# Optimization experiments

Measured on AMD Instinct MI355X. Metric: run time of the kernel, lower is better.

The kernel has to match this reference:

```python
import jax, jax.numpy as jnp
import numpy as np

B, N, H, NH = 1024, 101, 128, 8
HD = H // NH
EPS = 1e-5  # torch LayerNorm default


def _xavier(k, shape):
    fan_in, fan_out = shape
    lim = float(np.sqrt(6.0 / (fan_in + fan_out)))
    return jax.random.uniform(k, shape, jnp.float32, -lim, lim)


def setup_inputs() -> dict:
    key = jax.random.key(0)
    ks = jax.random.split(key, 12)
    return {
        "encoder_inputs": jax.random.normal(ks[0], (B, N, H), jnp.float32),
        "pool": jax.random.normal(ks[1], (B, H), jnp.float32),
        "capacity": jnp.ones((B, 1), jnp.float32),
        "demand": jax.random.uniform(ks[2], (B, N), jnp.float32),
        "fc_w": _xavier(ks[3], (H + 1, H)),      # nn.Linear(hidden+1, hidden, bias=False), stored [in,out]
        "fc1_w": _xavier(ks[4], (H, H)),
        "dec_ln_g": jnp.ones((H,), jnp.float32),
        "dec_ln_b": jnp.zeros((H,), jnp.float32),
        "wq": _xavier(ks[5], (H, H)),             # TransformerAttention q/k/v/out projections
        "wk": _xavier(ks[6], (H, H)),
        "wv": _xavier(ks[7], (H, H)),
        "wo": _xavier(ks[8], (H, H)),
        "kp_w": _xavier(ks[9], (H, H)),           # pointer self.k
        "ptr_ln_g": jnp.ones((H,), jnp.float32),
        "ptr_ln_b": jnp.zeros((H,), jnp.float32),
        "n_steps": 120,
        "T": 1,
        "greedy": 1,
    }


def _ln(x, g, b):
    mu = x.mean(-1, keepdims=True)
    v = ((x - mu) ** 2).mean(-1, keepdims=True)
    return (x - mu) * jax.lax.rsqrt(v + EPS) * g + b


def _forward(encoder_inputs, pool, capacity, demand, fc_w, fc1_w, dec_ln_g, dec_ln_b,
             wq, wk, wv, wo, kp_w, ptr_ln_g, ptr_ln_b, n_steps, T):
    b, n, h = encoder_inputs.shape
    # context projections are loop-invariant -> hoist out of the decode loop
    Kh = (encoder_inputs @ wk).reshape(b, n, NH, HD)
    Vh = (encoder_inputs @ wv).reshape(b, n, NH, HD)
    Kp = encoder_inputs @ kp_w            # [B,N,H] pointer keys
    pool_proc = pool @ fc1_w              # [B,H]
    ar = jnp.arange(n)
    arB = jnp.arange(b)
    inv_sqrt_hd = 1.0 / jnp.sqrt(jnp.float32(HD))
    inv_sqrt_h = 1.0 / jnp.sqrt(jnp.float32(h))

    def step(carry, i):
        mask1, cap, idx, inp = carry
        # decoder input: fc([emb, remaining_cap]) + fc1(pool), LayerNorm
        d = jnp.concatenate([inp, cap], -1) @ fc_w + pool_proc
        d = _ln(d, dec_ln_g, dec_ln_b)
        # ---- update_mask ----
        hit = (ar[None, :] == idx[:, None]) & (idx[:, None] != 0)
        mask1 = jnp.where((i > 0) & hit, 1.0, mask1)
        infeas = (mask1[:, 1:] > 0) | (demand[:, 1:] > cap)      # customers
        any_feas = jnp.any(~infeas, axis=-1)
        depot_m = jnp.where(i == 0, True, (idx == 0) & any_feas)  # mask depot if at depot & feasible cust exists
        all_cust = jnp.all(infeas, axis=-1)
        depot_m = jnp.where(all_cust, False, depot_m)             # only depot allowed if no feasible customer
        mb = jnp.concatenate([depot_m[:, None], infeas], axis=1)  # [B,N] bool, True = masked
        # ---- TransformerAttention (mhalayer) ----
        Qh = (d @ wq).reshape(b, NH, HD)
        logit = jnp.einsum('bhd,bnhd->bhn', Qh, Kh) * inv_sqrt_hd
        logit = jnp.where(mb[:, None, :], -jnp.inf, logit)
        attn = jax.nn.softmax(logit, axis=-1)
        x = jnp.einsum('bhn,bnhd->bhd', attn, Vh).reshape(b, h) @ wo
        # ---- pointer compatibility ----
        xn = _ln(x, ptr_ln_g, ptr_ln_b)
        comp = jnp.einsum('bh,bnh->bn', xn, Kp) * inv_sqrt_h
        comp = jnp.where(mb, -jnp.inf, comp)
        comp = jnp.where(jnp.all(mb, axis=-1, keepdims=True), 0.0, comp)
        p = jax.nn.softmax(comp / T, axis=-1) + 1e-10
        p = p / p.sum(axis=-1, keepdims=True)
        idx = jnp.argmax(p, axis=-1)                              # greedy selection
        lp = jnp.log(jnp.take_along_axis(p, idx[:, None], 1)[:, 0])
        done = mask1[:, 1:].sum(-1) >= (n - 1)
        lp = jnp.where(done, 0.0, lp)
        # ---- update_state (demand lookups via .item() in torch -> stop_gradient) ----
        sel = jax.lax.stop_gradient(jnp.take_along_axis(demand, idx[:, None], 1))
        cap = jnp.where(idx[:, None] == 0, jax.lax.stop_gradient(capacity), cap - sel)
        inp = encoder_inputs[arB, idx]
        return (mask1, cap, idx, inp), (idx, lp)

    init = (jnp.zeros((b, n), jnp.float32), capacity,
            jnp.zeros((b,), jnp.int32), encoder_inputs[:, 0])
    _, (idxs, lps) = jax.lax.scan(step, init, jnp.arange(n_steps))
    last = idxs[-1]
    final = jnp.where(last == 0, -1, 0).astype(jnp.int32)
    actions = jnp.concatenate(
        [jnp.zeros((b, 1), jnp.int32), idxs.T.astype(jnp.int32), final[:, None]], axis=1)
    log_p = lps.sum(0)
    return actions, log_p


def reference(encoder_inputs, pool, capacity, demand, fc_w, fc1_w, dec_ln_g, dec_ln_b,
              wq, wk, wv, wo, kp_w, ptr_ln_g, ptr_ln_b, n_steps, T, greedy):
    # greedy flag: this reference implements the greedy=True path (deterministic argmax).
    return _forward(encoder_inputs, pool, capacity, demand, fc_w, fc1_w, dec_ln_g,
                    dec_ln_b, wq, wk, wv, wo, kp_w, ptr_ln_g, ptr_ln_b,
                    int(n_steps), float(T))
```

## Files before the change

kernel.cpp:

```cpp
#include <hip/hip_runtime.h>
#include <math.h>

constexpr int N_ = 101, H_ = 128;
constexpr int SKE = 132;
constexpr float EPS_ = 1e-5f;

constexpr int OFF_TAB = 0;
constexpr int OFF_AT  = N_ * SKE;
constexpr int OFF_FC  = OFF_AT + 816;
constexpr int OFF_XV  = OFF_FC + 128;
constexpr int OFF_YR  = OFF_XV + 128;
constexpr int OFF_CP  = OFF_YR + 128;
constexpr int LDS_WORDS = OFF_CP + 128;

__device__ __forceinline__ float rdlane(float v, int l) {
  return __int_as_float(__builtin_amdgcn_readlane(__float_as_int(v), l));
}

template<int CTRL, int RM>
__device__ __forceinline__ float dppadd(float x) {
  int v = __builtin_amdgcn_update_dpp(0, __float_as_int(x), CTRL, RM, 0xf, true);
  return x + __int_as_float(v);
}
template<int CTRL, int RM>
__device__ __forceinline__ float dppmax(float x) {
  int v = __builtin_amdgcn_update_dpp(__float_as_int(x), __float_as_int(x), CTRL, RM, 0xf, false);
  return fmaxf(x, __int_as_float(v));
}
__device__ __forceinline__ float wave_sum(float x) {
  x = dppadd<0x111,0xf>(x);
  x = dppadd<0x112,0xf>(x);
  x = dppadd<0x114,0xf>(x);
  x = dppadd<0x118,0xf>(x);
  x = dppadd<0x142,0xa>(x);
  x = dppadd<0x143,0xc>(x);
  return rdlane(x, 63);
}
__device__ __forceinline__ float wave_max(float x) {
  x = dppmax<0x111,0xf>(x); x = dppmax<0x112,0xf>(x);
  x = dppmax<0x114,0xf>(x); x = dppmax<0x118,0xf>(x);
  x = dppmax<0x142,0xa>(x); x = dppmax<0x143,0xc>(x);
  return rdlane(x, 63);
}
__device__ __forceinline__ float grp4_sum(float x) {
  x = dppadd<0x111,0xf>(x);
  x = dppadd<0x112,0xf>(x);
  return x;
}

__global__ __launch_bounds__(512, 2) void gat_decoder(
    const float* __restrict__ enc, const float* __restrict__ pool,
    const float* __restrict__ capac, const float* __restrict__ dem,
    const float* __restrict__ fcw, const float* __restrict__ fc1w,
    const float* __restrict__ lng, const float* __restrict__ lnb,
    const float* __restrict__ wq, const float* __restrict__ wk,
    const float* __restrict__ wvm, const float* __restrict__ wo,
    const float* __restrict__ kpw, const float* __restrict__ plg,
    const float* __restrict__ plb, const int* __restrict__ tp,
    float* __restrict__ out, int Bv, int ns)
{
  __shared__ float sm[LDS_WORDS];
  const int tid  = threadIdx.x;
  const int b    = blockIdx.x;
  const int lane = tid & 63;
  const int wvid = tid >> 6;
  const int sl   = lane & 3;
  const int lc   = lane >> 2;
  const int col  = wvid * 16 + lc;
  const int n1 = lane, n2 = lane + 64;

  const float NEG_INF = -__builtin_inff();
  int ti = tp[0];
  float Tf = (ti > 1000000 || ti < -1000000) ? __int_as_float((int)ti) : (float)ti;
  const float inv_sqrt_h = 1.0f / sqrtf(128.0f);
  const float PSUM_CONST = 1.0f + (float)N_ * 1e-10f;

  const float* encb = enc + (size_t)b * (N_ * H_);

  float* TAB = sm + OFF_TAB;  float* AT = sm + OFF_AT;
  float* FC  = sm + OFF_FC;   float* XV = sm + OFF_XV;
  float* YR  = sm + OFF_YR;   float* CP = sm + OFF_CP;

  const int j3 = tid & 127;
  const int g3 = __builtin_amdgcn_readfirstlane(tid >> 7);
  const int r03 = g3 * 26, nr3 = (g3 == 3) ? 23 : 26;

  {
    const float* pb = pool + (size_t)b * H_;
    float p = 0.f;
    #pragma unroll
    for (int r = 0; r < 32; ++r) p = fmaf(pb[g3 * 32 + r], fc1w[(g3 * 32 + r) * H_ + j3], p);
    AT[g3 * 128 + j3] = p;
    if (tid < 128) FC[tid] = fcw[128 * H_ + tid];
  }
  __syncthreads();
  if (tid < 128) CP[tid] = AT[tid] + AT[128 + tid] + AT[256 + tid] + AT[384 + tid];

  {
    float acc[26];
    #pragma unroll
    for (int t = 0; t < 26; ++t) acc[t] = 0.f;
    for (int k0 = 0; k0 < H_; k0 += 8) {
      float w8[8];
      #pragma unroll
      for (int kk = 0; kk < 8; ++kk) w8[kk] = kpw[(k0 + kk) * H_ + j3];
      #pragma unroll
      for (int t = 0; t < 26; ++t) if (t < nr3) {
        const float* ep = encb + (r03 + t) * H_ + k0;
        #pragma unroll
        for (int kk = 0; kk < 8; ++kk) acc[t] = fmaf(ep[kk], w8[kk], acc[t]);
      }
    }
    #pragma unroll
    for (int t = 0; t < 26; ++t) if (t < nr3) TAB[(r03 + t) * SKE + j3] = acc[t];
  }
  __syncthreads();

  float kpT[32], kps, cpb;
  {
    const int neff = (col < N_) ? col : (N_ - 1);
    const float* src = TAB + neff * SKE + sl * 32;
    float ks = 0.f, cb = 0.f;
    #pragma unroll
    for (int r = 0; r < 32; ++r) {
      const float kv = src[r];
      const float pg = plg[sl * 32 + r];
      const float pb2 = plb[sl * 32 + r];
      ks = fmaf(kv, pg, ks);
      cb = fmaf(kv, pb2, cb);
      kpT[r] = kv * pg;
    }
    kps = grp4_sum(ks); cpb = grp4_sum(cb);
  }
  __syncthreads();

  {
    float acc[26];
    #pragma unroll
    for (int t = 0; t < 26; ++t) acc[t] = 0.f;
    for (int k0 = 0; k0 < H_; k0 += 8) {
      float w8[8];
      #pragma unroll
      for (int kk = 0; kk < 8; ++kk) w8[kk] = wk[(k0 + kk) * H_ + j3];
      #pragma unroll
      for (int t = 0; t < 26; ++t) if (t < nr3) {
        const float* ep = encb + (r03 + t) * H_ + k0;
        #pragma unroll
        for (int kk = 0; kk < 8; ++kk) acc[t] = fmaf(ep[kk], w8[kk], acc[t]);
      }
    }
    #pragma unroll
    for (int t = 0; t < 26; ++t) if (t < nr3) TAB[(r03 + t) * SKE + j3] = acc[t];
  }
  __syncthreads();

  float khA[16], khB[16];
  {
    const int row2 = (n2 < N_) ? n2 : n1;
    const float* s1 = TAB + n1 * SKE + wvid * 16;
    const float* s2 = TAB + row2 * SKE + wvid * 16;
    #pragma unroll
    for (int d = 0; d < 16; ++d) { khA[d] = s1[d]; khB[d] = s2[d]; }
  }
  __syncthreads();

  {
    const float pcj = CP[j3];
    float acc[26];
    #pragma unroll
    for (int t = 0; t < 26; ++t) acc[t] = pcj;
    for (int k0 = 0; k0 < H_; k0 += 8) {
      float w8[8];
      #pragma unroll
      for (int kk = 0; kk < 8; ++kk) w8[kk] = fcw[(k0 + kk) * H_ + j3];
      #pragma unroll
      for (int t = 0; t < 26; ++t) if (t < nr3) {
        const float* ep = encb + (r03 + t) * H_ + k0;
        #pragma unroll
        for (int kk = 0; kk < 8; ++kk) acc[t] = fmaf(ep[kk], w8[kk], acc[t]);
      }
    }
    #pragma unroll
    for (int t = 0; t < 26; ++t) if (t < nr3) TAB[(r03 + t) * SKE + j3] = acc[t];
  }

  float vh[26];
  {
    const int r0v = sl * 26, nrv = (sl == 3) ? 23 : 26;
    #pragma unroll
    for (int t = 0; t < 26; ++t) vh[t] = 0.f;
    for (int k0 = 0; k0 < H_; k0 += 8) {
      float w8[8];
      #pragma unroll
      for (int kk = 0; kk < 8; ++kk) w8[kk] = wvm[(k0 + kk) * H_ + col];
      #pragma unroll
      for (int t = 0; t < 26; ++t) if (t < nrv) {
        const float* ep = encb + (r0v + t) * H_ + k0;
        #pragma unroll
        for (int kk = 0; kk < 8; ++kk) vh[t] = fmaf(ep[kk], w8[kk], vh[t]);
      }
    }
  }
  float wq_r[32], wo_r[32], wqs, qb, wfc;
  {
    float ws = 0.f, bsum = 0.f, wf = 0.f;
    #pragma unroll
    for (int r = 0; r < 32; ++r) {
      wo_r[r] = wo[(sl * 32 + r) * H_ + col];
      const float w = wq[(sl * 32 + r) * H_ + col];
      const float lg = lng[sl * 32 + r];
      const float lb = lnb[sl * 32 + r];
      const float wp = w * lg;
      wq_r[r] = wp;
      ws += wp;
      bsum = fmaf(w, lb, bsum);
      wf = fmaf(wp, fcw[128 * H_ + sl * 32 + r], wf);
    }
    wqs = grp4_sum(ws); qb = grp4_sum(bsum); wfc = grp4_sum(wf);
  }
  const float capv = capac[b];
  float cap = capv, lpsum = 0.f;
  float demA = dem[(size_t)b * N_ + n1];
  float demC = (n2 < N_) ? dem[(size_t)b * N_ + n2] : 0.f;
  int vis = 0, pidx = 0;
  bool m1a = false, m1c = false, mbA, mbB;
  {
    bool infA = (n1 >= 1) && (demA > cap);
    bool infB = (n2 >= N_) || (demC > cap);
    bool feasA = (n1 >= 1) && !infA;
    bool feasB = (n2 < N_) && !infB;
    const bool anyf = __any(feasA || feasB);
    mbA = (n1 == 0) ? anyf : infA;
    mbB = infB;
  }
  __syncthreads();

  for (int i = 0; i < ns; ++i) {
    const int pu = __builtin_amdgcn_readfirstlane(pidx);
    const float* EROW = TAB + pu * SKE;

    {
      const float DA = EROW[n1] + cap * FC[n1];
      const float DC = EROW[n2 & 127] + cap * FC[n2 & 127];
      const float mu = wave_sum(DA + DC) * (1.f / 128.f);
      const float da = DA - mu, dc = DC - mu;
      const float inv = 1.0f / sqrtf(wave_sum(da * da + dc * dc) * (1.f / 128.f) + EPS_);
      const float4* e4 = (const float4*)(EROW + sl * 32);
      float p = 0.f;
      #pragma unroll
      for (int r4 = 0; r4 < 8; ++r4) {
        const float4 u = e4[r4];
        p = fmaf(wq_r[r4 * 4 + 0], u.x, p);
        p = fmaf(wq_r[r4 * 4 + 1], u.y, p);
        p = fmaf(wq_r[r4 * 4 + 2], u.z, p);
        p = fmaf(wq_r[r4 * 4 + 3], u.w, p);
      }
      p = grp4_sum(p);
      const float q = inv * ((p + cap * wfc) - mu * wqs) + qb;
      float a1 = 0.f, a2r = 0.f;
      #pragma unroll
      for (int d = 0; d < 16; ++d) {
        const float qdv = rdlane(q, 4 * d + 3);
        a1  = fmaf(qdv, khA[d], a1);
        a2r = fmaf(qdv, khB[d], a2r);
      }
      a1 = mbA ? NEG_INF : a1 * 0.25f;
      float a2 = (n2 < N_ && !mbB) ? a2r * 0.25f : NEG_INF;
      const float mx = wave_max(fmaxf(a1, a2));
      float e1 = expf(a1 - mx);
      float e2 = (n2 < N_) ? expf(a2 - mx) : 0.f;
      const float ss = wave_sum(e1 + e2);
      AT[wvid * N_ + n1] = e1 / ss;
      if (n2 < N_) AT[wvid * N_ + n2] = e2 / ss;
      const float* aw = AT + wvid * N_ + sl * 26;
      const int nrv = (sl == 3) ? 23 : 26;
      float x = 0.f;
      #pragma unroll
      for (int t = 0; t < 26; ++t) if (t < nrv) x = fmaf(aw[t], vh[t], x);
      x = grp4_sum(x);
      if (sl == 3) XV[col] = x;
    }
    __syncthreads();

    {
      const float4* xp4 = (const float4*)(XV + sl * 32);
      float y = 0.f;
      #pragma unroll
      for (int r4 = 0; r4 < 8; ++r4) {
        const float4 u = xp4[r4];
        y = fmaf(wo_r[r4 * 4 + 0], u.x, y);
        y = fmaf(wo_r[r4 * 4 + 1], u.y, y);
        y = fmaf(wo_r[r4 * 4 + 2], u.z, y);
        y = fmaf(wo_r[r4 * 4 + 3], u.w, y);
      }
      y = grp4_sum(y);
      if (sl == 3) YR[col] = y;
    }
    __syncthreads();

    {
      const float YA = YR[n1], YC = YR[n2 & 127];
      const float mu = wave_sum(YA + YC) * (1.f / 128.f);
      const float da = YA - mu, dc = YC - mu;
      const float inv = 1.0f / sqrtf(wave_sum(da * da + dc * dc) * (1.f / 128.f) + EPS_);
      const float4* yp4 = (const float4*)(YR + sl * 32);
      float c = 0.f;
      #pragma unroll
      for (int r4 = 0; r4 < 8; ++r4) {
        const float4 u = yp4[r4];
        c = fmaf(kpT[r4 * 4 + 0], u.x, c);
        c = fmaf(kpT[r4 * 4 + 1], u.y, c);
        c = fmaf(kpT[r4 * 4 + 2], u.z, c);
        c = fmaf(kpT[r4 * 4 + 3], u.w, c);
      }
      c = grp4_sum(c);
      const float comp = inv * (c - mu * kps) + cpb;
      if (sl == 3 && col < N_) CP[col] = comp;
    }
    __syncthreads();

    {
      const bool allmb = __all(mbA && mbB);
      float c1 = mbA ? NEG_INF : CP[n1] * inv_sqrt_h / Tf;
      float c2 = (n2 < N_ && !mbB) ? CP[n2 & 127] * inv_sqrt_h / Tf : NEG_INF;
      if (allmb) { c1 = 0.f; c2 = (n2 < N_) ? 0.f : NEG_INF; }
      const float mx = wave_max(fmaxf(c1, c2));
      const unsigned long long b1 = __ballot(c1 == mx);
      const unsigned long long b2 = __ballot(c2 == mx);
      const int bis = b1 ? (__ffsll((long long)b1) - 1)
                         : (64 + __ffsll((long long)b2) - 1);
      float e1 = expf(c1 - mx);
      float e2 = (n2 < N_) ? expf(c2 - mx) : 0.f;
      const float ss = wave_sum(e1 + e2);
      float lp = logf((1.0f / ss + 1e-10f) / PSUM_CONST);
      if (vis >= N_ - 1) lp = 0.f;
      lpsum += lp;
      const float dsel = (bis < 64) ? rdlane(demA, bis) : rdlane(demC, bis - 64);
      cap = (bis == 0) ? capv : (cap - dsel);
      if (bis != 0) {
        const bool newly = ((bis == n1) && !m1a) || ((bis == n2) && !m1c);
        if (__any(newly)) vis += 1;
        m1a = m1a || (bis == n1);
        m1c = m1c || (bis == n2);
      }
      bool infA = (n1 >= 1) && (m1a || demA > cap);
      bool infB = (n2 >= N_) || m1c || (demC > cap);
      bool feasA = (n1 >= 1) && !infA;
      bool feasB = (n2 < N_) && !infB;
      const bool anyf = __any(feasA || feasB);
      const bool depot_m = anyf && (bis == 0);
      mbA = (n1 == 0) ? depot_m : infA;
      mbB = infB;
      pidx = bis;
      if (wvid == 0 && lane == 0) out[(size_t)b * (ns + 2) + 1 + i] = (float)bis;
    }
  }

  if (wvid == 0 && lane == 0) {
    out[(size_t)b * (ns + 2)] = 0.f;
    out[(size_t)b * (ns + 2) + ns + 1] = (pidx == 0) ? -1.f : 0.f;
    out[(size_t)Bv * (ns + 2) + b] = lpsum;
  }
}

extern "C" void kernel_launch(void* const* d_in, const int* in_sizes, int n_in,
                              void* d_out, int out_size, void* d_ws, size_t ws_size,
                              hipStream_t stream) {
  const int Bv = in_sizes[0] / (N_ * H_);
  const int ns = out_size / Bv - 3;
  gat_decoder<<<dim3(Bv), dim3(512), 0, stream>>>(
      (const float*)d_in[0],  (const float*)d_in[1],  (const float*)d_in[2],
      (const float*)d_in[3],  (const float*)d_in[4],  (const float*)d_in[5],
      (const float*)d_in[6],  (const float*)d_in[7],  (const float*)d_in[8],
      (const float*)d_in[9],  (const float*)d_in[10], (const float*)d_in[11],
      (const float*)d_in[12], (const float*)d_in[13], (const float*)d_in[14],
      (const int*)d_in[16],
      (float*)d_out, Bv, ns);
}
```

Measured before the change: 2.903 ms.

## Precompute per-node query projections and LayerNorm stats, keep keys in LDS

Before the decode loop, the kernel now computes the fc-projected embeddings times wq*gamma for every node and stores the result in LDS. It also precomputes per-row sum, sum-of-squares and dot-with-fc statistics, so each step's decoder LayerNorm and query projection become a few table lookups instead of wave reductions plus a 32-wide dot product. Head keys are read from LDS each step instead of being held in registers, and the XV/YR buffers get a padded swizzle to avoid bank conflicts. LDS use grows to about 110 KB of dynamic shared memory, which may limit blocks per CU, and computing variance as E[x^2]-mu^2 risks cancellation error.

```diff
diff --git a/kernel.cpp b/kernel.cpp
--- a/kernel.cpp
+++ b/kernel.cpp
@@ -2,21 +2,21 @@
 #include <math.h>
 
 constexpr int N_ = 101, H_ = 128;
-constexpr int SKE = 132;
 constexpr float EPS_ = 1e-5f;
 
-constexpr int OFF_TAB = 0;
-constexpr int OFF_AT  = N_ * SKE;
-constexpr int OFF_FC  = OFF_AT + 816;
-constexpr int OFF_XV  = OFF_FC + 128;
-constexpr int OFF_YR  = OFF_XV + 128;
-constexpr int OFF_CP  = OFF_YR + 128;
-constexpr int LDS_WORDS = OFF_CP + 128;
+constexpr int OFF_QEF = 0;
+constexpr int OFF_KT  = 12928;
+constexpr int OFF_AT  = 25960;
+constexpr int OFF_XV  = 26776;
+constexpr int OFF_YR  = 26920;
+constexpr int OFF_CP  = 27064;
+constexpr int OFF_RS  = 27192;
+constexpr int LDS_WORDS = 27512;
+constexpr int LDS_BYTES = LDS_WORDS * 4;
 
 __device__ __forceinline__ float rdlane(float v, int l) {
   return __int_as_float(__builtin_amdgcn_readlane(__float_as_int(v), l));
 }
-
 template<int CTRL, int RM>
 __device__ __forceinline__ float dppadd(float x) {
   int v = __builtin_amdgcn_update_dpp(0, __float_as_int(x), CTRL, RM, 0xf, true);
@@ -28,12 +28,9 @@
   return fmaxf(x, __int_as_float(v));
 }
 __device__ __forceinline__ float wave_sum(float x) {
-  x = dppadd<0x111,0xf>(x);
-  x = dppadd<0x112,0xf>(x);
-  x = dppadd<0x114,0xf>(x);
-  x = dppadd<0x118,0xf>(x);
-  x = dppadd<0x142,0xa>(x);
-  x = dppadd<0x143,0xc>(x);
+  x = dppadd<0x111,0xf>(x); x = dppadd<0x112,0xf>(x);
+  x = dppadd<0x114,0xf>(x); x = dppadd<0x118,0xf>(x);
+  x = dppadd<0x142,0xa>(x); x = dppadd<0x143,0xc>(x);
   return rdlane(x, 63);
 }
 __device__ __forceinline__ float wave_max(float x) {
@@ -47,6 +44,7 @@
   x = dppadd<0x112,0xf>(x);
   return x;
 }
+__device__ __forceinline__ int swz(int k) { return (k >> 5) * 36 + (k & 31); }
 
 __global__ __launch_bounds__(512, 2) void gat_decoder(
     const float* __restrict__ enc, const float* __restrict__ pool,
@@ -59,7 +57,7 @@
     const float* __restrict__ plb, const int* __restrict__ tp,
     float* __restrict__ out, int Bv, int ns)
 {
-  __shared__ float sm[LDS_WORDS];
+  extern __shared__ float sm[];
   const int tid  = threadIdx.x;
   const int b    = blockIdx.x;
   const int lane = tid & 63;
@@ -77,9 +75,10 @@
 
   const float* encb = enc + (size_t)b * (N_ * H_);
 
-  float* TAB = sm + OFF_TAB;  float* AT = sm + OFF_AT;
-  float* FC  = sm + OFF_FC;   float* XV = sm + OFF_XV;
-  float* YR  = sm + OFF_YR;   float* CP = sm + OFF_CP;
+  float* QEF = sm + OFF_QEF; float* KT = sm + OFF_KT;
+  float* AT = sm + OFF_AT;   float* XVp = sm + OFF_XV;
+  float* YRp = sm + OFF_YR;  float* CP = sm + OFF_CP;
+  float* RS = sm + OFF_RS;
 
   const int j3 = tid & 127;
   const int g3 = __builtin_amdgcn_readfirstlane(tid >> 7);
@@ -91,11 +90,7 @@
     #pragma unroll
     for (int r = 0; r < 32; ++r) p = fmaf(pb[g3 * 32 + r], fc1w[(g3 * 32 + r) * H_ + j3], p);
     AT[g3 * 128 + j3] = p;
-    if (tid < 128) FC[tid] = fcw[128 * H_ + tid];
-  }
-  __syncthreads();
-  if (tid < 128) CP[tid] = AT[tid] + AT[128 + tid] + AT[256 + tid] + AT[384 + tid];
-
+  }
   {
     float acc[26];
     #pragma unroll
@@ -112,14 +107,15 @@
       }
     }
     #pragma unroll
-    for (int t = 0; t < 26; ++t) if (t < nr3) TAB[(r03 + t) * SKE + j3] = acc[t];
-  }
-  __syncthreads();
-
+    for (int t = 0; t < 26; ++t) if (t < nr3) KT[(r03 + t) * 129 + j3] = acc[t];
+  }
+  __syncthreads();
+
+  if (tid < 128) CP[tid] = AT[tid] + AT[128 + tid] + AT[256 + tid] + AT[384 + tid];
   float kpT[32], kps, cpb;
   {
     const int neff = (col < N_) ? col : (N_ - 1);
-    const float* src = TAB + neff * SKE + sl * 32;
+    const float* src = KT + neff * 129 + sl * 32;
     float ks = 0.f, cb = 0.f;
     #pragma unroll
     for (int r = 0; r < 32; ++r) {
@@ -135,13 +131,14 @@
   __syncthreads();
 
   {
+    const float pcj = CP[j3];
     float acc[26];
     #pragma unroll
-    for (int t = 0; t < 26; ++t) acc[t] = 0.f;
-    for (int k0 = 0; k0 < H_; k0 += 8) {
-      float w8[8];
-      #pragma unroll
-      for (int kk = 0; kk < 8; ++kk) w8[kk] = wk[(k0 + kk) * H_ + j3];
+    for (int t = 0; t < 26; ++t) acc[t] = pcj;
+    for (int k0 = 0; k0 < H_; k0 += 8) {
+      float w8[8];
+      #pragma unroll
+      for (int kk = 0; kk < 8; ++kk) w8[kk] = fcw[(k0 + kk) * H_ + j3];
       #pragma unroll
       for (int t = 0; t < 26; ++t) if (t < nr3) {
         const float* ep = encb + (r03 + t) * H_ + k0;
@@ -150,29 +147,50 @@
       }
     }
     #pragma unroll
-    for (int t = 0; t < 26; ++t) if (t < nr3) TAB[(r03 + t) * SKE + j3] = acc[t];
-  }
-  __syncthreads();
-
-  float khA[16], khB[16];
-  {
-    const int row2 = (n2 < N_) ? n2 : n1;
-    const float* s1 = TAB + n1 * SKE + wvid * 16;
-    const float* s2 = TAB + row2 * SKE + wvid * 16;
-    #pragma unroll
-    for (int d = 0; d < 16; ++d) { khA[d] = s1[d]; khB[d] = s2[d]; }
-  }
-  __syncthreads();
-
-  {
-    const float pcj = CP[j3];
+    for (int t = 0; t < 26; ++t) if (t < nr3) KT[(r03 + t) * 129 + j3] = acc[t];
+  }
+  __syncthreads();
+
+  {
+    float qacc[26];
+    #pragma unroll
+    for (int t = 0; t < 26; ++t) qacc[t] = 0.f;
+    for (int k0 = 0; k0 < H_; k0 += 8) {
+      float w8[8];
+      #pragma unroll
+      for (int kk = 0; kk < 8; ++kk) w8[kk] = wq[(k0 + kk) * H_ + j3] * lng[k0 + kk];
+      #pragma unroll
+      for (int t = 0; t < 26; ++t) if (t < nr3) {
+        const float* erow = KT + (r03 + t) * 129 + k0;
+        #pragma unroll
+        for (int kk = 0; kk < 8; ++kk) qacc[t] = fmaf(erow[kk], w8[kk], qacc[t]);
+      }
+    }
+    #pragma unroll
+    for (int t = 0; t < 26; ++t) if (t < nr3) QEF[(r03 + t) * 128 + j3] = qacc[t];
+  }
+  if (tid < N_) {
+    const float* base = KT + tid * 129;
+    float s = 0.f, s2 = 0.f, sf = 0.f, fs = 0.f, fs2 = 0.f;
+    for (int r = 0; r < 128; ++r) {
+      const float v = base[r];
+      const float fr = fcw[128 * H_ + r];
+      s += v; s2 = fmaf(v, v, s2); sf = fmaf(v, fr, sf);
+      fs += fr; fs2 = fmaf(fr, fr, fs2);
+    }
+    RS[tid] = s; RS[104 + tid] = s2; RS[208 + tid] = sf;
+    if (tid == 0) { RS[312] = fs; RS[313] = fs2; }
+  }
+  __syncthreads();
+
+  {
     float acc[26];
     #pragma unroll
-    for (int t = 0; t < 26; ++t) acc[t] = pcj;
-    for (int k0 = 0; k0 < H_; k0 += 8) {
-      float w8[8];
-      #pragma unroll
-      for (int kk = 0; kk < 8; ++kk) w8[kk] = fcw[(k0 + kk) * H_ + j3];
+    for (int t = 0; t < 26; ++t) acc[t] = 0.f;
+    for (int k0 = 0; k0 < H_; k0 += 8) {
+      float w8[8];
+      #pragma unroll
+      for (int kk = 0; kk < 8; ++kk) w8[kk] = wk[(k0 + kk) * H_ + j3];
       #pragma unroll
       for (int t = 0; t < 26; ++t) if (t < nr3) {
         const float* ep = encb + (r03 + t) * H_ + k0;
@@ -181,9 +199,8 @@
       }
     }
     #pragma unroll
-    for (int t = 0; t < 26; ++t) if (t < nr3) TAB[(r03 + t) * SKE + j3] = acc[t];
-  }
-
+    for (int t = 0; t < 26; ++t) if (t < nr3) KT[(r03 + t) * 129 + j3] = acc[t];
+  }
   float vh[26];
   {
     const int r0v = sl * 26, nrv = (sl == 3) ? 23 : 26;
@@ -201,22 +218,16 @@
       }
     }
   }
-  float wq_r[32], wo_r[32], wqs, qb, wfc;
-  {
-    float ws = 0.f, bsum = 0.f, wf = 0.f;
-    #pragma unroll
-    for (int r = 0; r < 32; ++r) {
-      wo_r[r] = wo[(sl * 32 + r) * H_ + col];
-      const float w = wq[(sl * 32 + r) * H_ + col];
-      const float lg = lng[sl * 32 + r];
-      const float lb = lnb[sl * 32 + r];
-      const float wp = w * lg;
-      wq_r[r] = wp;
-      ws += wp;
-      bsum = fmaf(w, lb, bsum);
-      wf = fmaf(wp, fcw[128 * H_ + sl * 32 + r], wf);
-    }
-    wqs = grp4_sum(ws); qb = grp4_sum(bsum); wfc = grp4_sum(wf);
+  float wo_r[32];
+  #pragma unroll
+  for (int r = 0; r < 32; ++r) wo_r[r] = wo[(sl * 32 + r) * H_ + col];
+  float wqs = 0.f, qb = 0.f, wfc = 0.f;
+  for (int r = 0; r < 128; ++r) {
+    const float w = wq[r * H_ + col];
+    const float lg = lng[r], lb = lnb[r], fr = fcw[128 * H_ + r];
+    wqs = fmaf(w, lg, wqs);
+    qb  = fmaf(w, lb, qb);
+    wfc = fmaf(w * lg, fr, wfc);
   }
   const float capv = capac[b];
   float cap = capv, lpsum = 0.f;
@@ -234,35 +245,26 @@
     mbB = infB;
   }
   __syncthreads();
+  const float fcsum = RS[312], fcs2 = RS[313];
 
   for (int i = 0; i < ns; ++i) {
     const int pu = __builtin_amdgcn_readfirstlane(pidx);
-    const float* EROW = TAB + pu * SKE;
 
     {
-      const float DA = EROW[n1] + cap * FC[n1];
-      const float DC = EROW[n2 & 127] + cap * FC[n2 & 127];
-      const float mu = wave_sum(DA + DC) * (1.f / 128.f);
-      const float da = DA - mu, dc = DC - mu;
-      const float inv = 1.0f / sqrtf(wave_sum(da * da + dc * dc) * (1.f / 128.f) + EPS_);
-      const float4* e4 = (const float4*)(EROW + sl * 32);
-      float p = 0.f;
-      #pragma unroll
-      for (int r4 = 0; r4 < 8; ++r4) {
-        const float4 u = e4[r4];
-        p = fmaf(wq_r[r4 * 4 + 0], u.x, p);
-        p = fmaf(wq_r[r4 * 4 + 1], u.y, p);
-        p = fmaf(wq_r[r4 * 4 + 2], u.z, p);
-        p = fmaf(wq_r[r4 * 4 + 3], u.w, p);
-      }
-      p = grp4_sum(p);
-      const float q = inv * ((p + cap * wfc) - mu * wqs) + qb;
+      const float efsum = RS[pu], efs2 = RS[104 + pu], effc = RS[208 + pu];
+      const float mu = (efsum + cap * fcsum) * (1.f / 128.f);
+      const float msq = (efs2 + 2.f * cap * effc + cap * cap * fcs2) * (1.f / 128.f);
+      const float inv = 1.0f / sqrtf(msq - mu * mu + EPS_);
+      const float qefv = QEF[pu * 128 + col];
+      const float q = inv * (qefv + cap * wfc - mu * wqs) + qb;
+      const float* kb1 = KT + n1 * 129 + wvid * 16;
+      const float* kb2 = KT + ((n2 < N_) ? n2 : n1) * 129 + wvid * 16;
       float a1 = 0.f, a2r = 0.f;
       #pragma unroll
       for (int d = 0; d < 16; ++d) {
-        const float qdv = rdlane(q, 4 * d + 3);
-        a1  = fmaf(qdv, khA[d], a1);
-        a2r = fmaf(qdv, khB[d], a2r);
+        const float qdv = rdlane(q, 4 * d);
+        a1  = fmaf(qdv, kb1[d], a1);
+        a2r = fmaf(qdv, kb2[d], a2r);
       }
       a1 = mbA ? NEG_INF : a1 * 0.25f;
       float a2 = (n2 < N_ && !mbB) ? a2r * 0.25f : NEG_INF;
@@ -278,12 +280,12 @@
       #pragma unroll
       for (int t = 0; t < 26; ++t) if (t < nrv) x = fmaf(aw[t], vh[t], x);
       x = grp4_sum(x);
-      if (sl == 3) XV[col] = x;
+      if (sl == 3) XVp[swz(col)] = x;
     }
     __syncthreads();
 
     {
-      const float4* xp4 = (const float4*)(XV + sl * 32);
+      const float4* xp4 = (const float4*)(XVp + sl * 36);
       float y = 0.f;
       #pragma unroll
       for (int r4 = 0; r4 < 8; ++r4) {
@@ -294,16 +296,16 @@
         y = fmaf(wo_r[r4 * 4 + 3], u.w, y);
       }
       y = grp4_sum(y);
-      if (sl == 3) YR[col] = y;
+      if (sl == 3) YRp[swz(col)] = y;
     }
     __syncthreads();
 
     {
-      const float YA = YR[n1], YC = YR[n2 & 127];
+      const float YA = YRp[swz(n1)], YC = YRp[swz(n2 & 127)];
       const float mu = wave_sum(YA + YC) * (1.f / 128.f);
       const float da = YA - mu, dc = YC - mu;
       const float inv = 1.0f / sqrtf(wave_sum(da * da + dc * dc) * (1.f / 128.f) + EPS_);
-      const float4* yp4 = (const float4*)(YR + sl * 32);
+      const float4* yp4 = (const float4*)(YRp + sl * 36);
       float c = 0.f;
       #pragma unroll
       for (int r4 = 0; r4 < 8; ++r4) {
@@ -368,7 +370,9 @@
                               hipStream_t stream) {
   const int Bv = in_sizes[0] / (N_ * H_);
   const int ns = out_size / Bv - 3;
-  gat_decoder<<<dim3(Bv), dim3(512), 0, stream>>>(
+  (void)hipFuncSetAttribute(reinterpret_cast<const void*>(gat_decoder),
+                            hipFuncAttributeMaxDynamicSharedMemorySize, LDS_BYTES);
+  gat_decoder<<<dim3(Bv), dim3(512), LDS_BYTES, stream>>>(
       (const float*)d_in[0],  (const float*)d_in[1],  (const float*)d_in[2],
       (const float*)d_in[3],  (const float*)d_in[4],  (const float*)d_in[5],
       (const float*)d_in[6],  (const float*)d_in[7],  (const float*)d_in[8],
```

Result: no change. 2.911 ms, median of 2 (+0.3%).
